# Optimization experiments

Hardware: AMD Instinct MI355X
Metric: run time of the kernel (lower is better)

Reference implementation:

```python
import jax, jax.numpy as jnp
import numpy as np

# module hyper-params (from init_kwargs)
NMS_THRESHOLD = 0.45
CLASSES = 32        # number of classes to filter
PRE_THRESHOLD = 0.005
FIRST_CLASS = 0

B, N, C = 8, 2048, 32  # batch, boxes-per-image, total class channels


def setup_inputs() -> dict:
    key = jax.random.key(0)
    k1, k2, k3 = jax.random.split(key, 3)
    # boxes in (x1, y1, x2, y2) corner format with positive extent
    cxy = jax.random.uniform(k1, (B, N, 2), dtype=jnp.float32) * 100.0
    wh = jax.random.uniform(k2, (B, N, 2), dtype=jnp.float32) * 20.0 + 1.0
    bbs = jnp.concatenate([cxy - wh * 0.5, cxy + wh * 0.5], axis=-1)  # [B,N,4]
    conf = jax.random.uniform(k3, (B, C, N), dtype=jnp.float32)       # [B,C,N]
    return {"bbs": bbs, "conf": conf}


def _iou_matrix(boxes):
    # boxes: [N,4] (x1,y1,x2,y2) -> pairwise IoU [N,N]
    lt = jnp.maximum(boxes[:, None, :2], boxes[None, :, :2])
    rb = jnp.minimum(boxes[:, None, 2:], boxes[None, :, 2:])
    wh = jnp.clip(rb - lt, 0.0)
    inter = wh[..., 0] * wh[..., 1]
    area = (boxes[:, 2] - boxes[:, 0]) * (boxes[:, 3] - boxes[:, 1])
    union = area[:, None] + area[None, :] - inter
    return inter / jnp.maximum(union, jnp.float32(1e-12))


def _nms_one_class(iou, conf_c):
    # iou: [N,N] pairwise IoU for this image; conf_c: [N] confidences of one class.
    # Greedy NMS in descending confidence order; suppressed boxes get conf 0.
    if PRE_THRESHOLD > 0:
        conf_c = jnp.where(conf_c > PRE_THRESHOLD, conf_c, 0.0)
    order = jnp.argsort(-conf_c)          # descending
    conf_s = conf_c[order]                # sorted confidences
    idx = jnp.arange(N)

    def step(suppressed, i):
        # suppressed[i] is final at step i (only earlier steps could set it)
        active = (~suppressed[i]) & (conf_s[i] > 0)
        row = iou[order[i]][order]        # IoU of box i (sorted order) vs all, sorted
        suppressed = suppressed | (active & (row > NMS_THRESHOLD) & (idx > i))
        return suppressed, suppressed[i] if False else suppressed[i]

    def step2(suppressed, i):
        sup_i = suppressed[i]
        active = (~sup_i) & (conf_s[i] > 0)
        row = iou[order[i]][order]
        new_sup = suppressed | (active & (row > NMS_THRESHOLD) & (idx > i))
        return new_sup, sup_i

    _, sup_at = jax.lax.scan(step2, jnp.zeros((N,), dtype=bool), idx)
    out_s = jnp.where(sup_at, 0.0, conf_s)
    return jnp.zeros((N,), conf_c.dtype).at[order].set(out_s)


def reference(bbs, conf):
    # bbs [B,N,4], conf [B,C,N] -> filtered conf [B,C,N]
    iou = jax.vmap(_iou_matrix)(bbs)  # [B,N,N]
    nms_bc = jax.vmap(lambda io, cf: jax.vmap(lambda c: _nms_one_class(io, c))(cf))(iou, conf)
    cls = jnp.arange(conf.shape[1])
    in_range = (cls >= FIRST_CLASS) & (cls < FIRST_CLASS + CLASSES)
    # classes outside [first_class, first_class+classes) pass through unchanged
    return jnp.where(in_range[None, :, None], nms_bc, conf)
```

## Files before the change

### kernel.cpp

```cpp
#include <hip/hip_runtime.h>
#include <stdint.h>

#pragma clang fp contract(off)

#define BB   8
#define NN   2048
#define CC   32
#define WORDS 64
#define NBLK 64
#define NMS_THR 0.45f
#define PRE_THR 0.005f
#define PADI(i) ((((i) >> 5) * 33) + ((i) & 31))
#define KPAD(i) ((i) + ((i) >> 4))

typedef unsigned long long u64;

__global__ __launch_bounds__(256) void adj_kernel(const float* __restrict__ bbs,
                                                  uint32_t* __restrict__ adj) {
    __shared__ float sx1[2112], sy1[2112], sx2[2112], sy2[2112];
    const int b = blockIdx.y;
    const int t = threadIdx.x;
    const float4* bp = (const float4*)bbs + (size_t)b * NN;
    for (int i = t; i < NN; i += 256) {
        float4 v = bp[i];
        int p = PADI(i);
        sx1[p] = v.x; sy1[p] = v.y; sx2[p] = v.z; sy2[p] = v.w;
    }
    __syncthreads();

    const int wave = t >> 6, lane = t & 63;
    const int row0 = blockIdx.x * 16 + wave * 4;
    const float THI = 0.45f * 1.00002f;
    const float TLO = 0.45f * 0.99998f;

    float ax1[4], ay1[4], ax2[4], ay2[4], areaA[4];
#pragma unroll
    for (int r = 0; r < 4; ++r) {
        int p = PADI(row0 + r);
        ax1[r] = sx1[p]; ay1[r] = sy1[p]; ax2[r] = sx2[p]; ay2[r] = sy2[p];
        areaA[r] = (ax2[r] - ax1[r]) * (ay2[r] - ay1[r]);
    }
    uint32_t w[4] = {0, 0, 0, 0};
#pragma unroll 4
    for (int j = 0; j < 32; ++j) {
        int p = lane * 33 + j;
        float bx1 = sx1[p], by1 = sy1[p], bx2 = sx2[p], by2 = sy2[p];
        float areaB = (bx2 - bx1) * (by2 - by1);
#pragma unroll
        for (int r = 0; r < 4; ++r) {
            float ltx = fmaxf(ax1[r], bx1), lty = fmaxf(ay1[r], by1);
            float rbx = fminf(ax2[r], bx2), rby = fminf(ay2[r], by2);
            float ww = fmaxf(rbx - ltx, 0.0f);
            float hh = fmaxf(rby - lty, 0.0f);
            float inter = ww * hh;
            float uni  = (areaA[r] + areaB) - inter;
            float unim = fmaxf(uni, 1e-12f);
            float q1 = inter * __builtin_amdgcn_rcpf(unim);
            bool hi = q1 > THI;
            bool lo = q1 < TLO;
            bool adjb;
            if (__builtin_expect(__any((int)!(hi || lo)), 0))
                adjb = (inter / unim) > NMS_THR;
            else
                adjb = hi;
            if (adjb) w[r] |= (1u << j);
        }
    }
#pragma unroll
    for (int r = 0; r < 4; ++r) {
        int row = row0 + r;
        uint32_t dmask = (lane == (row >> 5)) ? ~(1u << (row & 31)) : 0xFFFFFFFFu;
        adj[((size_t)b * NN + row) * WORDS + lane] = w[r] & dmask;
    }
}

__device__ __forceinline__ void ce_reg(u64& a, u64& b, bool up) {
    u64 mn = (a < b) ? a : b;
    u64 mx = (a < b) ? b : a;
    a = up ? mx : mn;
    b = up ? mn : mx;
}

__global__ __launch_bounds__(1024) void sort_kernel(const float* __restrict__ conf,
                                                    uint32_t* __restrict__ wsOrd) {
    __shared__ u64 keys[2176];
    const int bc = blockIdx.x;
    const int t  = threadIdx.x;
    const float* cf = conf + (size_t)bc * NN;

    if (t < 512) {
        const int g = 4 * t;
        float4 v = ((const float4*)cf)[t];
        float f0 = (v.x > PRE_THR) ? v.x : 0.0f;
        float f1 = (v.y > PRE_THR) ? v.y : 0.0f;
        float f2 = (v.z > PRE_THR) ? v.z : 0.0f;
        float f3 = (v.w > PRE_THR) ? v.w : 0.0f;
        u64 a0 = ((u64)__float_as_uint(f0) << 32) | (uint32_t)(NN - 1 - (g + 0));
        u64 a1 = ((u64)__float_as_uint(f1) << 32) | (uint32_t)(NN - 1 - (g + 1));
        u64 a2 = ((u64)__float_as_uint(f2) << 32) | (uint32_t)(NN - 1 - (g + 2));
        u64 a3 = ((u64)__float_as_uint(f3) << 32) | (uint32_t)(NN - 1 - (g + 3));
        ce_reg(a0, a1, true);
        ce_reg(a2, a3, false);
        bool up4 = ((g & 4) == 0);
        ce_reg(a0, a2, up4); ce_reg(a1, a3, up4);
        ce_reg(a0, a1, up4); ce_reg(a2, a3, up4);
        keys[KPAD(g + 0)] = a0; keys[KPAD(g + 1)] = a1;
        keys[KPAD(g + 2)] = a2; keys[KPAD(g + 3)] = a3;
    }
    __syncthreads();

    for (unsigned k = 8; k <= NN; k <<= 1) {
        unsigned j = k >> 1;
        while (j >= 2) {
            const unsigned h = j >> 1;
            if (t < 512) {
                unsigned g  = (((unsigned)t & ~(h - 1)) << 2) | ((unsigned)t & (h - 1));
                bool up = ((g & k) == 0);
                u64 e0 = keys[KPAD(g)];
                u64 e1 = keys[KPAD(g + h)];
                u64 e2 = keys[KPAD(g + j)];
                u64 e3 = keys[KPAD(g + j + h)];
                ce_reg(e0, e2, up); ce_reg(e1, e3, up);
                ce_reg(e0, e1, up); ce_reg(e2, e3, up);
                keys[KPAD(g)]         = e0;
                keys[KPAD(g + h)]     = e1;
                keys[KPAD(g + j)]     = e2;
                keys[KPAD(g + j + h)] = e3;
            }
            __syncthreads();
            j >>= 2;
        }
        if (j == 1) {
            unsigned i  = (unsigned)t << 1;
            bool up = ((i & k) == 0);
            u64 a = keys[KPAD(i)], d = keys[KPAD(i + 1)];
            ce_reg(a, d, up);
            keys[KPAD(i)] = a; keys[KPAD(i + 1)] = d;
            __syncthreads();
        }
    }

    uint32_t* ov = wsOrd + (size_t)bc * NN;
    for (int r = t; r < NN; r += 1024) {
        u64 kk = keys[KPAD(r)];
        uint32_t idx = (uint32_t)(NN - 1) - (uint32_t)(kk & 0xffffffffu);
        uint32_t nz  = ((uint32_t)(kk >> 32) != 0u) ? 0x10000u : 0u;
        ov[r] = idx | nz;
    }
}

__global__ __launch_bounds__(256) void extract_kernel(const uint32_t* __restrict__ adj,
                                                      const uint32_t* __restrict__ wsOrd,
                                                      uint32_t* __restrict__ wsM) {
    const int blkid = blockIdx.x;
    const int bc = blkid >> 3, chunk = blkid & 7;
    const int b  = bc >> 5;
    const int t = threadIdx.x, wv = t >> 6, lane = t & 63, e = lane & 31, h = lane >> 5;
    const uint32_t* ov = wsOrd + (size_t)bc * NN;
    const uint32_t* ab = adj + (size_t)b * NN * WORDS;

    for (int blk = chunk * 8 + wv; blk < chunk * 8 + 8; blk += 4) {
        uint32_t ue = ov[blk * 32 + e];
        int widx = (int)((ue & 0xffffu) >> 5);
        int bpos = (int)(ue & 31u);
        uint32_t wb[16];
#pragma unroll
        for (int k = 0; k < 16; ++k) {
            uint32_t ud = ov[blk * 32 + k * 2 + h] & 0xffffu;
            wb[k] = ab[(size_t)ud * WORDS + widx];
        }
        uint32_t vM = 0;
#pragma unroll
        for (int k = 0; k < 16; ++k) {
            unsigned long long bal = __ballot(((wb[k] >> bpos) & 1u) != 0u);
            vM = (lane == 2 * k    ) ? (uint32_t)bal         : vM;
            vM = (lane == 2 * k + 1) ? (uint32_t)(bal >> 32) : vM;
        }
        if (lane < 32)
            wsM[(size_t)bc * NN + blk * 32 + lane] = vM & (0xFFFFFFFEu << lane);
    }
}

#define PREFETCH_ROWS(u_, r_)                                          \
  {                                                                    \
    _Pragma("unroll")                                                  \
    for (int d = 0; d < 32; ++d) {                                     \
      int ud_ = __builtin_amdgcn_readlane((int)(u_), d) & 0xffff;      \
      r_[d] = rowp[(size_t)ud_ * WORDS];                               \
    }                                                                  \
  }

#define RESOLVE(u_, m_, r_)                                            \
  {                                                                    \
    int wq_ = (int)((((u_) & 0xffffu) >> 5) << 2);                     \
    int pm_ = __builtin_amdgcn_ds_bpermute(wq_, (int)S);               \
    bool a0_ = ((((u_) >> 16) & 1u) != 0u) &&                          \
               (((pm_ >> ((u_) & 31u)) & 1) == 0);                     \
    uint32_t alive_ = (uint32_t)__ballot((int)a0_);                    \
    _Pragma("unroll")                                                  \
    for (int d = 0; d < 32; ++d) {                                     \
      uint32_t md_ = (uint32_t)__builtin_amdgcn_readlane((int)(m_), d);\
      alive_ = (alive_ & (1u << d)) ? (alive_ & ~md_) : alive_;        \
    }                                                                  \
    uint32_t acc_ = 0;                                                 \
    _Pragma("unroll")                                                  \
    for (int d = 0; d < 32; ++d)                                       \
      acc_ |= (alive_ & (1u << d)) ? r_[d] : 0u;                       \
    S |= acc_;                                                         \
  }

__global__ __launch_bounds__(64, 1) void scan_kernel(const float* __restrict__ conf,
                                                     const uint32_t* __restrict__ adj,
                                                     const uint32_t* __restrict__ wsOrd,
                                                     const uint32_t* __restrict__ wsM,
                                                     float* __restrict__ out) {
    __shared__ uint32_t ordL[NN];
    __shared__ uint32_t Ml[NN];
    __shared__ uint32_t Sarr[WORDS];
    const int bc = blockIdx.x;
    const int b  = bc >> 5;
    const int lane = threadIdx.x;
    const uint32_t* ov = wsOrd + (size_t)bc * NN;
    const uint32_t* mv = wsM   + (size_t)bc * NN;
    const uint32_t* const rowp = adj + (size_t)b * NN * WORDS + lane;
    const float* cf = conf + (size_t)bc * NN;
    float* op = out + (size_t)bc * NN;

    for (int i = lane; i < NN / 4; i += 64) {
        ((uint4*)ordL)[i] = ((const uint4*)ov)[i];
        ((uint4*)Ml)[i]   = ((const uint4*)mv)[i];
    }
    __syncthreads();

    uint32_t S = 0;
    uint32_t rA[32], rB[32];
    uint32_t uA = ordL[lane & 31],        mA = Ml[lane & 31];
    uint32_t uB = ordL[32 + (lane & 31)], mB = Ml[32 + (lane & 31)];
    PREFETCH_ROWS(uA, rA);
    PREFETCH_ROWS(uB, rB);

    for (int blk = 0; blk < NBLK; blk += 2) {
        uint32_t uN = 0, mN = 0;
        if (blk + 2 < NBLK) {
            uN = ordL[(blk + 2) * 32 + (lane & 31)];
            mN = Ml[(blk + 2) * 32 + (lane & 31)];
        }
        RESOLVE(uA, mA, rA);
        if (blk + 2 < NBLK) { uA = uN; mA = mN; PREFETCH_ROWS(uA, rA); }

        uint32_t uN2 = 0, mN2 = 0;
        if (blk + 3 < NBLK) {
            uN2 = ordL[(blk + 3) * 32 + (lane & 31)];
            mN2 = Ml[(blk + 3) * 32 + (lane & 31)];
        }
        RESOLVE(uB, mB, rB);
        if (blk + 3 < NBLK) { uB = uN2; mB = mN2; PREFETCH_ROWS(uB, rB); }
    }

    Sarr[lane] = S;
    __syncthreads();

#pragma unroll
    for (int it = 0; it < 8; ++it) {
        int i4 = it * 256 + lane * 4;
        float4 v = ((const float4*)cf)[it * 64 + lane];
        uint32_t sw = Sarr[i4 >> 5];
        float4 o;
        o.x = (v.x > PRE_THR && !((sw >> ((i4 + 0) & 31)) & 1u)) ? v.x : 0.0f;
        o.y = (v.y > PRE_THR && !((sw >> ((i4 + 1) & 31)) & 1u)) ? v.y : 0.0f;
        o.z = (v.z > PRE_THR && !((sw >> ((i4 + 2) & 31)) & 1u)) ? v.z : 0.0f;
        o.w = (v.w > PRE_THR && !((sw >> ((i4 + 3) & 31)) & 1u)) ? v.w : 0.0f;
        ((float4*)op)[it * 64 + lane] = o;
    }
}

__global__ __launch_bounds__(256) void nms_fallback(const float* __restrict__ conf,
                                                    const uint32_t* __restrict__ adj,
                                                    float* __restrict__ out) {
    __shared__ unsigned long long keys[NN];
    __shared__ uint32_t ordv[NN];
    __shared__ uint32_t Mlds[NBLK * 32];
    __shared__ uint32_t Sarr[WORDS];
    const int bc = blockIdx.x;
    const int b  = bc >> 5;
    const int t  = threadIdx.x;
    const float* cf = conf + (size_t)bc * NN;
    const uint32_t* const abase = adj + (size_t)b * NN * WORDS;

    for (int i = t; i < NN; i += 256) {
        float v  = cf[i];
        float vt = (v > PRE_THR) ? v : 0.0f;
        keys[i] = ((unsigned long long)__float_as_uint(vt) << 32) | (uint32_t)(NN - 1 - i);
    }
    __syncthreads();
    for (unsigned k = 2; k <= NN; k <<= 1)
        for (unsigned j = k >> 1; j > 0; j >>= 1) {
            for (unsigned p = t; p < NN / 2; p += 256) {
                unsigned i  = ((p & ~(j - 1)) << 1) | (p & (j - 1));
                unsigned ij = i | j;
                unsigned long long a = keys[i], d = keys[ij];
                bool up = ((i & k) == 0);
                if (up ? (a < d) : (a > d)) { keys[i] = d; keys[ij] = a; }
            }
            __syncthreads();
        }
    for (int r = t; r < NN; r += 256) {
        unsigned long long kk = keys[r];
        uint32_t idx = (uint32_t)(NN - 1) - (uint32_t)(kk & 0xffffffffu);
        uint32_t nz  = ((uint32_t)(kk >> 32) != 0u) ? 0x10000u : 0u;
        ordv[r] = idx | nz;
    }
    __syncthreads();
    {
        const int wid = t >> 6, lane = t & 63, e = lane & 31, h = lane >> 5;
        for (int blk = wid * 16; blk < wid * 16 + 16; ++blk) {
            uint32_t ue = ordv[blk * 32 + e];
            int widx = (int)((ue & 0xffffu) >> 5);
            int bpos = (int)(ue & 31u);
            uint32_t vM = 0;
#pragma unroll
            for (int half = 0; half < 2; ++half) {
                uint32_t wbuf[8];
#pragma unroll
                for (int k = 0; k < 8; ++k) {
                    int d = half * 16 + k * 2 + h;
                    uint32_t ud = ordv[blk * 32 + d] & 0xffffu;
                    wbuf[k] = abase[(size_t)ud * WORDS + widx];
                }
#pragma unroll
                for (int k = 0; k < 8; ++k) {
                    int d0 = half * 16 + k * 2;
                    unsigned long long bal = __ballot(((wbuf[k] >> bpos) & 1u) != 0u);
                    vM = (lane == d0    ) ? (uint32_t)bal         : vM;
                    vM = (lane == d0 + 1) ? (uint32_t)(bal >> 32) : vM;
                }
            }
            if (lane < 32) Mlds[blk * 32 + lane] = vM;
        }
    }
    __syncthreads();
    if (t < 64) {
        const int lane = t;
        const uint32_t* const rowp = abase + lane;
        uint32_t S = 0;
        uint32_t rbA[32], rbB[32];
        uint32_t u_c, m_c, u_n, m_n;
        u_c = ordv[lane & 31];
        m_c = Mlds[lane & 31];
#pragma unroll
        for (int d = 0; d < 32; ++d) {
            int ud = __builtin_amdgcn_readlane((int)u_c, d) & 0xffff;
            rbA[d] = rowp[(size_t)ud * WORDS];
        }
        auto do_block = [&](int blk, uint32_t (&rbC)[32], uint32_t (&rbN)[32]) {
            u_n = 0; m_n = 0;
            if (blk < 63) {
                u_n = ordv[(blk + 1) * 32 + (lane & 31)];
                m_n = Mlds[(blk + 1) * 32 + (lane & 31)];
#pragma unroll
                for (int d = 0; d < 32; ++d) {
                    int ud = __builtin_amdgcn_readlane((int)u_n, d) & 0xffff;
                    rbN[d] = rowp[(size_t)ud * WORDS];
                }
            }
            int wq  = (int)(((u_c & 0xffffu) >> 5) << 2);
            int bpv = (int)(u_c & 31u);
            int pm  = __builtin_amdgcn_ds_bpermute(wq, (int)S);
            bool a0 = (((u_c >> 16) & 1u) != 0u) && (((pm >> bpv) & 1) == 0);
            uint32_t alive = (uint32_t)__ballot((int)a0);
#pragma unroll
            for (int d = 0; d < 32; ++d) {
                uint32_t rowd = (uint32_t)__builtin_amdgcn_readlane((int)m_c, d);
                uint32_t mk = rowd & (0xFFFFFFFEu << d);
                alive = (alive & (1u << d)) ? (alive & ~mk) : alive;
            }
            uint32_t acc = 0;
#pragma unroll
            for (int d = 0; d < 32; ++d)
                acc |= (alive & (1u << d)) ? rbC[d] : 0u;
            S |= acc;
            u_c = u_n; m_c = m_n;
        };
        for (int blk = 0; blk < 64; blk += 2) {
            do_block(blk,     rbA, rbB);
            do_block(blk + 1, rbB, rbA);
        }
        Sarr[lane] = S;
    }
    __syncthreads();
    float* op = out + (size_t)bc * NN;
    for (int i = t; i < NN; i += 256) {
        float v = cf[i];
        bool sup = (Sarr[i >> 5] >> (i & 31)) & 1u;
        op[i] = (v > PRE_THR && !sup) ? v : 0.0f;
    }
}

extern "C" void kernel_launch(void* const* d_in, const int* in_sizes, int n_in,
                              void* d_out, int out_size, void* d_ws, size_t ws_size,
                              hipStream_t stream) {
    const float* bbs  = (const float*)d_in[0];
    const float* conf = (const float*)d_in[1];
    float* out = (float*)d_out;

    const size_t adjB = (size_t)BB * NN * WORDS * sizeof(uint32_t);
    const size_t ordB = (size_t)BB * CC * NN * sizeof(uint32_t);
    const size_t mB   = ordB;
    uint32_t* adj = (uint32_t*)d_ws;

    if (ws_size >= adjB + ordB + mB) {
        uint32_t* wsOrd = (uint32_t*)((char*)d_ws + adjB);
        uint32_t* wsM   = (uint32_t*)((char*)d_ws + adjB + ordB);
        adj_kernel    <<<dim3(NN / 16, BB), 256, 0, stream>>>(bbs, adj);
        sort_kernel   <<<BB * CC, 1024, 0, stream>>>(conf, wsOrd);
        extract_kernel<<<BB * CC * 8, 256, 0, stream>>>(adj, wsOrd, wsM);
        scan_kernel   <<<BB * CC, 64, 0, stream>>>(conf, adj, wsOrd, wsM, out);
    } else if (ws_size >= adjB) {
        adj_kernel  <<<dim3(NN / 16, BB), 256, 0, stream>>>(bbs, adj);
        nms_fallback<<<BB * CC, 256, 0, stream>>>(conf, adj, out);
    }
}
```

Measured before the change: 177.3 us.

## Interleave two class scans per wavefront in NMS scan kernel

Each scan block now handles two (batch,class) pairs and interleaves their serial resolve steps with separate row prefetch buffers. The aim is to hide the latency of the dependent readlane/ballot chain and the adjacency row loads by giving the wave independent work from a second class. It halves the number of blocks (from 256 to 128 on a GPU with many CUs), doubles register use for the prefetch arrays and doubles LDS per block. That could cut occupancy and leave compute units idle.

After: 278.2 us. 56.9% more time.

```diff
diff --git a/kernel.cpp b/kernel.cpp
--- a/kernel.cpp
+++ b/kernel.cpp
@@ -181,32 +181,32 @@
     }
 }
 
-#define PREFETCH_ROWS(u_, r_)                                          \
-  {                                                                    \
-    _Pragma("unroll")                                                  \
-    for (int d = 0; d < 32; ++d) {                                     \
-      int ud_ = __builtin_amdgcn_readlane((int)(u_), d) & 0xffff;      \
-      r_[d] = rowp[(size_t)ud_ * WORDS];                               \
-    }                                                                  \
+#define PREF(u_, r_)                                                    \
+  {                                                                     \
+    _Pragma("unroll")                                                   \
+    for (int d = 0; d < 32; ++d) {                                      \
+      int ud_ = __builtin_amdgcn_readlane((int)(u_), d) & 0xffff;       \
+      r_[d] = rowp[(size_t)ud_ * WORDS];                                \
+    }                                                                   \
   }
 
-#define RESOLVE(u_, m_, r_)                                            \
-  {                                                                    \
-    int wq_ = (int)((((u_) & 0xffffu) >> 5) << 2);                     \
-    int pm_ = __builtin_amdgcn_ds_bpermute(wq_, (int)S);               \
-    bool a0_ = ((((u_) >> 16) & 1u) != 0u) &&                          \
-               (((pm_ >> ((u_) & 31u)) & 1) == 0);                     \
-    uint32_t alive_ = (uint32_t)__ballot((int)a0_);                    \
-    _Pragma("unroll")                                                  \
-    for (int d = 0; d < 32; ++d) {                                     \
-      uint32_t md_ = (uint32_t)__builtin_amdgcn_readlane((int)(m_), d);\
-      alive_ = (alive_ & (1u << d)) ? (alive_ & ~md_) : alive_;        \
-    }                                                                  \
-    uint32_t acc_ = 0;                                                 \
-    _Pragma("unroll")                                                  \
-    for (int d = 0; d < 32; ++d)                                       \
-      acc_ |= (alive_ & (1u << d)) ? r_[d] : 0u;                       \
-    S |= acc_;                                                         \
+#define RES(S_, u_, m_, r_)                                             \
+  {                                                                     \
+    int pm_ = __builtin_amdgcn_ds_bpermute(                             \
+        (int)((((u_) & 0xffffu) >> 5) << 2), (int)(S_));                \
+    bool a0_ = ((((u_) >> 16) & 1u) != 0u) &&                           \
+               (((pm_ >> ((u_) & 31u)) & 1) == 0);                      \
+    uint32_t alive_ = (uint32_t)__ballot((int)a0_);                     \
+    _Pragma("unroll")                                                   \
+    for (int d = 0; d < 32; ++d) {                                      \
+      uint32_t md_ = (uint32_t)__builtin_amdgcn_readlane((int)(m_), d); \
+      alive_ = (alive_ & (1u << d)) ? (alive_ & ~md_) : alive_;         \
+    }                                                                   \
+    uint32_t acc_ = 0;                                                  \
+    _Pragma("unroll")                                                   \
+    for (int d = 0; d < 32; ++d)                                        \
+      acc_ |= (alive_ & (1u << d)) ? r_[d] : 0u;                        \
+    S_ |= acc_;                                                         \
   }
 
 __global__ __launch_bounds__(64, 1) void scan_kernel(const float* __restrict__ conf,
@@ -214,63 +214,90 @@
                                                      const uint32_t* __restrict__ wsOrd,
                                                      const uint32_t* __restrict__ wsM,
                                                      float* __restrict__ out) {
-    __shared__ uint32_t ordL[NN];
-    __shared__ uint32_t Ml[NN];
-    __shared__ uint32_t Sarr[WORDS];
-    const int bc = blockIdx.x;
-    const int b  = bc >> 5;
+    __shared__ uint32_t ordLA[NN], MlA[NN];
+    __shared__ uint32_t ordLB[NN], MlB[NN];
+    __shared__ uint32_t SarrA[WORDS], SarrB[WORDS];
+    const int g  = blockIdx.x;
+    const int b  = g >> 4;
+    const int bc0 = b * CC + (g & 15) * 2;
+    const int bc1 = bc0 + 1;
     const int lane = threadIdx.x;
-    const uint32_t* ov = wsOrd + (size_t)bc * NN;
-    const uint32_t* mv = wsM   + (size_t)bc * NN;
+    const int lane31 = lane & 31;
     const uint32_t* const rowp = adj + (size_t)b * NN * WORDS + lane;
-    const float* cf = conf + (size_t)bc * NN;
-    float* op = out + (size_t)bc * NN;
-
-    for (int i = lane; i < NN / 4; i += 64) {
-        ((uint4*)ordL)[i] = ((const uint4*)ov)[i];
-        ((uint4*)Ml)[i]   = ((const uint4*)mv)[i];
-    }
-    __syncthreads();
-
-    uint32_t S = 0;
-    uint32_t rA[32], rB[32];
-    uint32_t uA = ordL[lane & 31],        mA = Ml[lane & 31];
-    uint32_t uB = ordL[32 + (lane & 31)], mB = Ml[32 + (lane & 31)];
-    PREFETCH_ROWS(uA, rA);
-    PREFETCH_ROWS(uB, rB);
-
-    for (int blk = 0; blk < NBLK; blk += 2) {
-        uint32_t uN = 0, mN = 0;
-        if (blk + 2 < NBLK) {
-            uN = ordL[(blk + 2) * 32 + (lane & 31)];
-            mN = Ml[(blk + 2) * 32 + (lane & 31)];
-        }
-        RESOLVE(uA, mA, rA);
-        if (blk + 2 < NBLK) { uA = uN; mA = mN; PREFETCH_ROWS(uA, rA); }
-
-        uint32_t uN2 = 0, mN2 = 0;
-        if (blk + 3 < NBLK) {
-            uN2 = ordL[(blk + 3) * 32 + (lane & 31)];
-            mN2 = Ml[(blk + 3) * 32 + (lane & 31)];
-        }
-        RESOLVE(uB, mB, rB);
-        if (blk + 3 < NBLK) { uB = uN2; mB = mN2; PREFETCH_ROWS(uB, rB); }
-    }
-
-    Sarr[lane] = S;
+    const float* cfA = conf + (size_t)bc0 * NN;
+    const float* cfB = conf + (size_t)bc1 * NN;
+    float* opA = out + (size_t)bc0 * NN;
+    float* opB = out + (size_t)bc1 * NN;
+
+    {
+        const uint4* oA = (const uint4*)(wsOrd + (size_t)bc0 * NN);
+        const uint4* oB = (const uint4*)(wsOrd + (size_t)bc1 * NN);
+        const uint4* mA = (const uint4*)(wsM   + (size_t)bc0 * NN);
+        const uint4* mB = (const uint4*)(wsM   + (size_t)bc1 * NN);
+        for (int i = lane; i < NN / 4; i += 64) {
+            ((uint4*)ordLA)[i] = oA[i];
+            ((uint4*)MlA)[i]   = mA[i];
+            ((uint4*)ordLB)[i] = oB[i];
+            ((uint4*)MlB)[i]   = mB[i];
+        }
+    }
+    __syncthreads();
+
+    uint32_t SA = 0, SB = 0;
+    uint32_t rA0[32], rA1[32], rB0[32], rB1[32];
+    uint32_t uA0 = ordLA[lane31],      mA0 = MlA[lane31];
+    uint32_t uA1 = ordLA[32 + lane31], mA1 = MlA[32 + lane31];
+    uint32_t uB0 = ordLB[lane31],      mB0 = MlB[lane31];
+    uint32_t uB1 = ordLB[32 + lane31], mB1 = MlB[32 + lane31];
+    PREF(uA0, rA0);
+    PREF(uB0, rB0);
+    PREF(uA1, rA1);
+    PREF(uB1, rB1);
+
+    for (int k = 0; k < NBLK; k += 2) {
+        int k2 = (k + 2 > 63) ? 63 : k + 2;
+        int k3 = (k + 3 > 63) ? 63 : k + 3;
+        uint32_t uNA = ordLA[k2 * 32 + lane31], mNA = MlA[k2 * 32 + lane31];
+        uint32_t uNB = ordLB[k2 * 32 + lane31], mNB = MlB[k2 * 32 + lane31];
+        RES(SA, uA0, mA0, rA0);
+        uA0 = uNA; mA0 = mNA; PREF(uA0, rA0);
+        RES(SB, uB0, mB0, rB0);
+        uB0 = uNB; mB0 = mNB; PREF(uB0, rB0);
+        uint32_t uNA1 = ordLA[k3 * 32 + lane31], mNA1 = MlA[k3 * 32 + lane31];
+        uint32_t uNB1 = ordLB[k3 * 32 + lane31], mNB1 = MlB[k3 * 32 + lane31];
+        RES(SA, uA1, mA1, rA1);
+        uA1 = uNA1; mA1 = mNA1; PREF(uA1, rA1);
+        RES(SB, uB1, mB1, rB1);
+        uB1 = uNB1; mB1 = mNB1; PREF(uB1, rB1);
+    }
+
+    SarrA[lane] = SA;
+    SarrB[lane] = SB;
     __syncthreads();
 
 #pragma unroll
     for (int it = 0; it < 8; ++it) {
         int i4 = it * 256 + lane * 4;
-        float4 v = ((const float4*)cf)[it * 64 + lane];
-        uint32_t sw = Sarr[i4 >> 5];
+        float4 v = ((const float4*)cfA)[it * 64 + lane];
+        uint32_t sw = SarrA[i4 >> 5];
         float4 o;
         o.x = (v.x > PRE_THR && !((sw >> ((i4 + 0) & 31)) & 1u)) ? v.x : 0.0f;
         o.y = (v.y > PRE_THR && !((sw >> ((i4 + 1) & 31)) & 1u)) ? v.y : 0.0f;
         o.z = (v.z > PRE_THR && !((sw >> ((i4 + 2) & 31)) & 1u)) ? v.z : 0.0f;
         o.w = (v.w > PRE_THR && !((sw >> ((i4 + 3) & 31)) & 1u)) ? v.w : 0.0f;
-        ((float4*)op)[it * 64 + lane] = o;
+        ((float4*)opA)[it * 64 + lane] = o;
+    }
+#pragma unroll
+    for (int it = 0; it < 8; ++it) {
+        int i4 = it * 256 + lane * 4;
+        float4 v = ((const float4*)cfB)[it * 64 + lane];
+        uint32_t sw = SarrB[i4 >> 5];
+        float4 o;
+        o.x = (v.x > PRE_THR && !((sw >> ((i4 + 0) & 31)) & 1u)) ? v.x : 0.0f;
+        o.y = (v.y > PRE_THR && !((sw >> ((i4 + 1) & 31)) & 1u)) ? v.y : 0.0f;
+        o.z = (v.z > PRE_THR && !((sw >> ((i4 + 2) & 31)) & 1u)) ? v.z : 0.0f;
+        o.w = (v.w > PRE_THR && !((sw >> ((i4 + 3) & 31)) & 1u)) ? v.w : 0.0f;
+        ((float4*)opB)[it * 64 + lane] = o;
     }
 }
 
@@ -414,7 +441,7 @@
         adj_kernel    <<<dim3(NN / 16, BB), 256, 0, stream>>>(bbs, adj);
         sort_kernel   <<<BB * CC, 1024, 0, stream>>>(conf, wsOrd);
         extract_kernel<<<BB * CC * 8, 256, 0, stream>>>(adj, wsOrd, wsM);
-        scan_kernel   <<<BB * CC, 64, 0, stream>>>(conf, adj, wsOrd, wsM, out);
+        scan_kernel   <<<BB * CC / 2, 64, 0, stream>>>(conf, adj, wsOrd, wsM, out);
     } else if (ws_size >= adjB) {
         adj_kernel  <<<dim3(NN / 16, BB), 256, 0, stream>>>(bbs, adj);
         nms_fallback<<<BB * CC, 256, 0, stream>>>(conf, adj, out);
```

## Fetch adjacency rows only for surviving boxes in NMS scan

Applied to the files above, without the earlier changes.

Replaces the double-buffered prefetch of all 32 adjacency rows per block with a per-block loop. It first resolves intra-block survivors by iterating only over set bits of the alive mask, then loads and ORs the rows of survivors only, four at a time. This cuts global loads and per-bit select work when few boxes survive, but puts the row fetches on the critical path with no prefetch overlap, so memory latency is exposed serially per block.

After: 265.5 us. 1.5x slower.

```diff
diff --git a/kernel.cpp b/kernel.cpp
--- a/kernel.cpp
+++ b/kernel.cpp
@@ -181,34 +181,6 @@
     }
 }
 
-#define PREFETCH_ROWS(u_, r_)                                          \
-  {                                                                    \
-    _Pragma("unroll")                                                  \
-    for (int d = 0; d < 32; ++d) {                                     \
-      int ud_ = __builtin_amdgcn_readlane((int)(u_), d) & 0xffff;      \
-      r_[d] = rowp[(size_t)ud_ * WORDS];                               \
-    }                                                                  \
-  }
-
-#define RESOLVE(u_, m_, r_)                                            \
-  {                                                                    \
-    int wq_ = (int)((((u_) & 0xffffu) >> 5) << 2);                     \
-    int pm_ = __builtin_amdgcn_ds_bpermute(wq_, (int)S);               \
-    bool a0_ = ((((u_) >> 16) & 1u) != 0u) &&                          \
-               (((pm_ >> ((u_) & 31u)) & 1) == 0);                     \
-    uint32_t alive_ = (uint32_t)__ballot((int)a0_);                    \
-    _Pragma("unroll")                                                  \
-    for (int d = 0; d < 32; ++d) {                                     \
-      uint32_t md_ = (uint32_t)__builtin_amdgcn_readlane((int)(m_), d);\
-      alive_ = (alive_ & (1u << d)) ? (alive_ & ~md_) : alive_;        \
-    }                                                                  \
-    uint32_t acc_ = 0;                                                 \
-    _Pragma("unroll")                                                  \
-    for (int d = 0; d < 32; ++d)                                       \
-      acc_ |= (alive_ & (1u << d)) ? r_[d] : 0u;                       \
-    S |= acc_;                                                         \
-  }
-
 __global__ __launch_bounds__(64, 1) void scan_kernel(const float* __restrict__ conf,
                                                      const uint32_t* __restrict__ adj,
                                                      const uint32_t* __restrict__ wsOrd,
@@ -220,6 +192,7 @@
     const int bc = blockIdx.x;
     const int b  = bc >> 5;
     const int lane = threadIdx.x;
+    const int lane31 = lane & 31;
     const uint32_t* ov = wsOrd + (size_t)bc * NN;
     const uint32_t* mv = wsM   + (size_t)bc * NN;
     const uint32_t* const rowp = adj + (size_t)b * NN * WORDS + lane;
@@ -233,28 +206,45 @@
     __syncthreads();
 
     uint32_t S = 0;
-    uint32_t rA[32], rB[32];
-    uint32_t uA = ordL[lane & 31],        mA = Ml[lane & 31];
-    uint32_t uB = ordL[32 + (lane & 31)], mB = Ml[32 + (lane & 31)];
-    PREFETCH_ROWS(uA, rA);
-    PREFETCH_ROWS(uB, rB);
-
-    for (int blk = 0; blk < NBLK; blk += 2) {
-        uint32_t uN = 0, mN = 0;
-        if (blk + 2 < NBLK) {
-            uN = ordL[(blk + 2) * 32 + (lane & 31)];
-            mN = Ml[(blk + 2) * 32 + (lane & 31)];
-        }
-        RESOLVE(uA, mA, rA);
-        if (blk + 2 < NBLK) { uA = uN; mA = mN; PREFETCH_ROWS(uA, rA); }
-
-        uint32_t uN2 = 0, mN2 = 0;
-        if (blk + 3 < NBLK) {
-            uN2 = ordL[(blk + 3) * 32 + (lane & 31)];
-            mN2 = Ml[(blk + 3) * 32 + (lane & 31)];
-        }
-        RESOLVE(uB, mB, rB);
-        if (blk + 3 < NBLK) { uB = uN2; mB = mN2; PREFETCH_ROWS(uB, rB); }
+    uint32_t u = ordL[lane31];
+    uint32_t m = Ml[lane31];
+
+    for (int k = 0; k < NBLK; ++k) {
+        int kn = (k + 1 > 63) ? 63 : k + 1;
+        uint32_t uN = ordL[kn * 32 + lane31];
+        uint32_t mN = Ml[kn * 32 + lane31];
+
+        int pm = __builtin_amdgcn_ds_bpermute(
+            (int)(((u & 0xffffu) >> 5) << 2), (int)S);
+        bool a0 = (((u >> 16) & 1u) != 0u) && (((pm >> (u & 31u)) & 1) == 0);
+        uint32_t alive = (uint32_t)__ballot((int)a0);
+
+        if (alive) {
+            uint32_t work = alive, surv = 0;
+            while (work) {
+                int d = __builtin_ctz(work);
+                surv |= (1u << d);
+                uint32_t md = (uint32_t)__builtin_amdgcn_readlane((int)m, d);
+                work &= ~(md | (1u << d));
+            }
+            uint32_t w2 = surv;
+            while (w2) {
+                int d0 = __builtin_ctz(w2); w2 &= w2 - 1;
+                int d1 = w2 ? __builtin_ctz(w2) : d0; if (w2) w2 &= w2 - 1;
+                int d2 = w2 ? __builtin_ctz(w2) : d0; if (w2) w2 &= w2 - 1;
+                int d3 = w2 ? __builtin_ctz(w2) : d0; if (w2) w2 &= w2 - 1;
+                int i0 = __builtin_amdgcn_readlane((int)u, d0) & 0xffff;
+                int i1 = __builtin_amdgcn_readlane((int)u, d1) & 0xffff;
+                int i2 = __builtin_amdgcn_readlane((int)u, d2) & 0xffff;
+                int i3 = __builtin_amdgcn_readlane((int)u, d3) & 0xffff;
+                uint32_t r0 = rowp[(size_t)i0 * WORDS];
+                uint32_t r1 = rowp[(size_t)i1 * WORDS];
+                uint32_t r2 = rowp[(size_t)i2 * WORDS];
+                uint32_t r3 = rowp[(size_t)i3 * WORDS];
+                S |= (r0 | r1) | (r2 | r3);
+            }
+        }
+        u = uN; m = mN;
     }
 
     Sarr[lane] = S;
```
